# Optimization experiments

Measured on AMD Instinct MI355X. Metric: run time of the kernel, lower is better.

The kernel has to match this reference:

```python
import jax, jax.numpy as jnp
import numpy as np

B, T, D, H = 32, 4096, 768, 1024
RHOS = np.linspace(0.1, 0.9, 5)
TAU = 1.0
EPS = 1e-5


def entmax15(x):
    # exact 1.5-entmax along last axis (Peters et al. 2019)
    x = x / 2.0
    x_srt = jnp.flip(jnp.sort(x, axis=-1), axis=-1)  # descending
    n = x.shape[-1]
    rho = jnp.arange(1, n + 1, dtype=x.dtype)
    mean = jnp.cumsum(x_srt, axis=-1) / rho
    mean_sq = jnp.cumsum(x_srt * x_srt, axis=-1) / rho
    ss = rho * (mean_sq - mean * mean)
    delta = (1.0 - ss) / rho
    tau = mean - jnp.sqrt(jnp.clip(delta, 0.0))
    support = jnp.sum(tau <= x_srt, axis=-1, keepdims=True)
    tau_star = jnp.take_along_axis(tau, support - 1, axis=-1)
    return jnp.clip(x - tau_star, 0.0) ** 2


def setup_inputs() -> dict:
    key = jax.random.key(0)
    ks = jax.random.split(key, 8)
    embeddings = jax.random.normal(ks[0], (B, T, D), dtype=jnp.float32)
    ids = jax.random.randint(ks[1], (B, T), 0, 32000)
    lengths = jax.random.randint(ks[2], (B,), T // 4, T + 1)
    attn = (jnp.arange(T)[None, :] < lengths[:, None]).astype(jnp.float32)
    ln_g = jnp.ones((D,), jnp.float32)
    ln_b = jnp.zeros((D,), jnp.float32)
    W1 = 0.02 * jax.random.normal(ks[3], (D, H), dtype=jnp.float32)
    b1 = jnp.zeros((H,), jnp.float32)
    W2 = 0.02 * jax.random.normal(ks[4], (H, 1), dtype=jnp.float32)
    b2 = jnp.zeros((1,), jnp.float32)
    return {"embeddings": embeddings, "attn": attn, "ln_g": ln_g, "ln_b": ln_b,
            "W1": W1, "b1": b1, "W2": W2, "b2": b2, "ids": ids}


def reference(embeddings, attn, ln_g, ln_b, W1, b1, W2, b2, ids):
    emb = embeddings * attn[..., None]                      # [B,T,D]
    mu = jnp.mean(emb, axis=-1, keepdims=True)
    var = jnp.mean((emb - mu) ** 2, axis=-1, keepdims=True)
    xn = (emb - mu) / jnp.sqrt(var + EPS) * ln_g + ln_b
    h1 = jax.nn.gelu(xn @ W1 + b1, approximate=False)       # torch F.gelu (erf)
    scores = (h1 @ W2 + b2)[..., 0]                         # [B,T]
    scores = jnp.where(attn == 0, -1e9, scores)
    z = entmax15(scores / TAU) * attn                       # [B,T]
    sorted_idx = jnp.argsort(-z, axis=-1)                   # descending
    inv_rank = jnp.argsort(sorted_idx, axis=-1)             # rank of each position
    t_eff = jnp.sum(attn, axis=-1)                          # [B]
    rhos = jnp.asarray(RHOS, dtype=z.dtype)                 # [R]
    k = jnp.maximum(1, jnp.floor(rhos[:, None] * t_eff[None, :])).astype(jnp.int32)  # [R,B]
    h = (inv_rank[None] < k[:, :, None]).astype(z.dtype) * attn[None]  # [R,B,T]
    g = jax.lax.stop_gradient(h - z[None]) + z[None]        # straight-through
    return jnp.concatenate([z[None], g], axis=0)            # [1+R, B, T]
```

## Files before the change

### kernel.cpp

```cpp
#include <hip/hip_runtime.h>
#include <math.h>

#define Bc 32
#define Tc 4096
#define Dc 768
#define Hc 1024
#define BTc (Bc*Tc)
#define PLANE 786432

typedef __bf16 bf16x8 __attribute__((ext_vector_type(8)));
typedef float f32x16 __attribute__((ext_vector_type(16)));

__device__ __forceinline__ float gelu_erf(float x) {
  return 0.5f * x * (1.0f + erff(x * 0.70710678118654752440f));
}
__device__ __forceinline__ unsigned bf16rne(float x) {
  unsigned u = __float_as_uint(x);
  return (u + 0x7FFFu + ((u >> 16) & 1u)) >> 16;
}
__device__ __forceinline__ void split3(float x, unsigned& h, unsigned& m, unsigned& l) {
  h = bf16rne(x);
  float r1 = x - __uint_as_float(h << 16);
  m = bf16rne(r1);
  float r2 = r1 - __uint_as_float(m << 16);
  l = bf16rne(r2);
}
__device__ __forceinline__ unsigned f2o(float f) {
  unsigned b = __float_as_uint(f);
  return (b & 0x80000000u) ? ~b : (b | 0x80000000u);
}
__device__ __forceinline__ float o2f(unsigned o) {
  unsigned b = (o & 0x80000000u) ? (o & 0x7FFFFFFFu) : ~o;
  return __uint_as_float(b);
}

__global__ __launch_bounds__(256) void w1_split_k(
    const float* __restrict__ W1, ushort* __restrict__ w1s) {
  int id = blockIdx.x * 256 + threadIdx.x;
  int n = id & 1023, kg = id >> 10;
  unsigned hs[8], ms[8], ls[8];
  #pragma unroll
  for (int j = 0; j < 8; j++) {
    float x = W1[(size_t)(kg * 8 + j) * Hc + n];
    split3(x, hs[j], ms[j], ls[j]);
  }
  size_t o = ((size_t)kg * 1024 + n) * 8;
  int4 ph, pm, pl;
  ph.x = (int)(hs[0] | (hs[1] << 16)); ph.y = (int)(hs[2] | (hs[3] << 16));
  ph.z = (int)(hs[4] | (hs[5] << 16)); ph.w = (int)(hs[6] | (hs[7] << 16));
  pm.x = (int)(ms[0] | (ms[1] << 16)); pm.y = (int)(ms[2] | (ms[3] << 16));
  pm.z = (int)(ms[4] | (ms[5] << 16)); pm.w = (int)(ms[6] | (ms[7] << 16));
  pl.x = (int)(ls[0] | (ls[1] << 16)); pl.y = (int)(ls[2] | (ls[3] << 16));
  pl.z = (int)(ls[4] | (ls[5] << 16)); pl.w = (int)(ls[6] | (ls[7] << 16));
  *(int4*)(w1s + o)             = ph;
  *(int4*)(w1s + o + PLANE)     = pm;
  *(int4*)(w1s + o + 2 * PLANE) = pl;
}

__global__ __launch_bounds__(256) void ln_stats_k(
    const float* __restrict__ emb, const float* __restrict__ attn,
    float* __restrict__ mu, float* __restrict__ rstd) {
  int row = blockIdx.x * 4 + (threadIdx.x >> 6);
  int lane = threadIdx.x & 63;
  float a = attn[row];
  const float4* e = (const float4*)(emb + (size_t)row * Dc);
  float4 v0 = e[lane], v1 = e[lane + 64], v2 = e[lane + 128];
  float x[12] = {v0.x*a, v0.y*a, v0.z*a, v0.w*a,
                 v1.x*a, v1.y*a, v1.z*a, v1.w*a,
                 v2.x*a, v2.y*a, v2.z*a, v2.w*a};
  float s = 0.f;
  #pragma unroll
  for (int i = 0; i < 12; i++) s += x[i];
  #pragma unroll
  for (int o = 32; o; o >>= 1) s += __shfl_xor(s, o);
  float m = s / 768.0f;
  float q = 0.f;
  #pragma unroll
  for (int i = 0; i < 12; i++) { float d = x[i] - m; q += d * d; }
  #pragma unroll
  for (int o = 32; o; o >>= 1) q += __shfl_xor(q, o);
  float var = q / 768.0f;
  if (lane == 0) { mu[row] = m; rstd[row] = 1.0f / sqrtf(var + 1e-5f); }
}

__global__ __launch_bounds__(512, 1) void gemm_scores_mfma10(
    const float* __restrict__ emb, const float* __restrict__ attn,
    const float* __restrict__ ln_g, const float* __restrict__ ln_b,
    const ushort* __restrict__ w1s, const float* __restrict__ b1,
    const float* __restrict__ W2, const float* __restrict__ b2,
    const float* __restrict__ mu, const float* __restrict__ rstd,
    float* __restrict__ spart) {
  __shared__ int4 Abuf[2][3][4][128];
  __shared__ float gls[768], bls[768];
  __shared__ float red[8][128];
  const int id = blockIdx.x;
  const int xcd = id & 7;
  const int y = xcd & 1;
  const int xg = (id >> 3) * 4 + (xcd >> 1);
  const int base = xg * 128;
  if (attn[base] == 0.0f) return;
  const int hbase = y * 512;
  const int t = threadIdx.x;
  const int lane = t & 63;
  const int lrow = lane & 31;
  const int lkg = lane >> 5;
  const int w = t >> 6;

  if (t < 192) {
    *(float4*)&gls[t * 4] = *(const float4*)&ln_g[t * 4];
    *(float4*)&bls[t * 4] = *(const float4*)&ln_b[t * 4];
  }
  const int srow = t & 127;
  const int skg = t >> 7;
  const int skoff = skg * 8;
  const float la  = attn[base + srow];
  const float lmu = mu[base + srow];
  const float lrs = rstd[base + srow];
  const float* erow = emb + (size_t)(base + srow) * Dc + skoff;

  f32x16 acc[8];
  #pragma unroll
  for (int nt = 0; nt < 8; nt++)
    #pragma unroll
    for (int r = 0; r < 16; r++) acc[nt][r] = 0.f;

  __syncthreads();
  {
    float4 e0 = *(const float4*)(erow);
    float4 e1 = *(const float4*)(erow + 4);
    float4 g0 = *(const float4*)&gls[skoff];
    float4 g1 = *(const float4*)&gls[skoff + 4];
    float4 q0 = *(const float4*)&bls[skoff];
    float4 q1 = *(const float4*)&bls[skoff + 4];
    float xs[8] = {e0.x,e0.y,e0.z,e0.w,e1.x,e1.y,e1.z,e1.w};
    float gs[8] = {g0.x,g0.y,g0.z,g0.w,g1.x,g1.y,g1.z,g1.w};
    float bs[8] = {q0.x,q0.y,q0.z,q0.w,q1.x,q1.y,q1.z,q1.w};
    unsigned hh[8], hm[8], hl[8];
    #pragma unroll
    for (int e = 0; e < 8; e++) {
      float xn = (xs[e] * la - lmu) * lrs * gs[e] + bs[e];
      split3(xn, hh[e], hm[e], hl[e]);
    }
    int4 ph, pm, pl;
    ph.x = (int)(hh[0] | (hh[1] << 16)); ph.y = (int)(hh[2] | (hh[3] << 16));
    ph.z = (int)(hh[4] | (hh[5] << 16)); ph.w = (int)(hh[6] | (hh[7] << 16));
    pm.x = (int)(hm[0] | (hm[1] << 16)); pm.y = (int)(hm[2] | (hm[3] << 16));
    pm.z = (int)(hm[4] | (hm[5] << 16)); pm.w = (int)(hm[6] | (hm[7] << 16));
    pl.x = (int)(hl[0] | (hl[1] << 16)); pl.y = (int)(hl[2] | (hl[3] << 16));
    pl.z = (int)(hl[4] | (hl[5] << 16)); pl.w = (int)(hl[6] | (hl[7] << 16));
    Abuf[0][0][skg][srow] = ph;
    Abuf[0][1][skg][srow] = pm;
    Abuf[0][2][skg][srow] = pl;
  }
  __syncthreads();

  const ushort* wbase = w1s + ((size_t)hbase + w * 64 + lrow) * 8;

  #pragma unroll 1
  for (int i = 0; i < 24; i++) {
    const int p = i & 1;
    const bool more = (i < 23);
    #pragma unroll
    for (int kh = 0; kh < 2; kh++) {
      const int kg = kh * 2 + lkg;
      const ushort* bp = wbase + (size_t)(i * 4 + kg) * 8192;
      bf16x8 Bh0 = *(const bf16x8*)(bp);
      bf16x8 Bh1 = *(const bf16x8*)(bp + 256);
      bf16x8 Bm0 = *(const bf16x8*)(bp + PLANE);
      bf16x8 Bm1 = *(const bf16x8*)(bp + PLANE + 256);
      bf16x8 Bl0 = *(const bf16x8*)(bp + 2 * PLANE);
      bf16x8 Bl1 = *(const bf16x8*)(bp + 2 * PLANE + 256);
      #pragma unroll
      for (int rt = 0; rt < 4; rt++) {
        bf16x8 a0 = *(const bf16x8*)&Abuf[p][0][kg][rt * 32 + lrow];
        bf16x8 a1 = *(const bf16x8*)&Abuf[p][1][kg][rt * 32 + lrow];
        bf16x8 a2 = *(const bf16x8*)&Abuf[p][2][kg][rt * 32 + lrow];
        f32x16* ac = acc + rt * 2;
        ac[0] = __builtin_amdgcn_mfma_f32_32x32x16_bf16(a0, Bh0, ac[0], 0, 0, 0);
        ac[1] = __builtin_amdgcn_mfma_f32_32x32x16_bf16(a0, Bh1, ac[1], 0, 0, 0);
        ac[0] = __builtin_amdgcn_mfma_f32_32x32x16_bf16(a0, Bm0, ac[0], 0, 0, 0);
        ac[1] = __builtin_amdgcn_mfma_f32_32x32x16_bf16(a0, Bm1, ac[1], 0, 0, 0);
        ac[0] = __builtin_amdgcn_mfma_f32_32x32x16_bf16(a1, Bh0, ac[0], 0, 0, 0);
        ac[1] = __builtin_amdgcn_mfma_f32_32x32x16_bf16(a1, Bh1, ac[1], 0, 0, 0);
        ac[0] = __builtin_amdgcn_mfma_f32_32x32x16_bf16(a1, Bm0, ac[0], 0, 0, 0);
        ac[1] = __builtin_amdgcn_mfma_f32_32x32x16_bf16(a1, Bm1, ac[1], 0, 0, 0);
        ac[0] = __builtin_amdgcn_mfma_f32_32x32x16_bf16(a0, Bl0, ac[0], 0, 0, 0);
        ac[1] = __builtin_amdgcn_mfma_f32_32x32x16_bf16(a0, Bl1, ac[1], 0, 0, 0);
        ac[0] = __builtin_amdgcn_mfma_f32_32x32x16_bf16(a2, Bh0, ac[0], 0, 0, 0);
        ac[1] = __builtin_amdgcn_mfma_f32_32x32x16_bf16(a2, Bh1, ac[1], 0, 0, 0);
      }
    }
    if (more) {
      const float* ep = erow + (i + 1) * 32;
      const int koff = (i + 1) * 32 + skoff;
      float4 e0 = *(const float4*)(ep);
      float4 e1 = *(const float4*)(ep + 4);
      float4 g0 = *(const float4*)&gls[koff];
      float4 g1 = *(const float4*)&gls[koff + 4];
      float4 q0 = *(const float4*)&bls[koff];
      float4 q1 = *(const float4*)&bls[koff + 4];
      float xs[8] = {e0.x,e0.y,e0.z,e0.w,e1.x,e1.y,e1.z,e1.w};
      float gs[8] = {g0.x,g0.y,g0.z,g0.w,g1.x,g1.y,g1.z,g1.w};
      float bs[8] = {q0.x,q0.y,q0.z,q0.w,q1.x,q1.y,q1.z,q1.w};
      unsigned hh[8], hm[8], hl[8];
      #pragma unroll
      for (int e = 0; e < 8; e++) {
        float xn = (xs[e] * la - lmu) * lrs * gs[e] + bs[e];
        split3(xn, hh[e], hm[e], hl[e]);
      }
      int4 ph, pm, pl;
      ph.x = (int)(hh[0] | (hh[1] << 16)); ph.y = (int)(hh[2] | (hh[3] << 16));
      ph.z = (int)(hh[4] | (hh[5] << 16)); ph.w = (int)(hh[6] | (hh[7] << 16));
      pm.x = (int)(hm[0] | (hm[1] << 16)); pm.y = (int)(hm[2] | (hm[3] << 16));
      pm.z = (int)(hm[4] | (hm[5] << 16)); pm.w = (int)(hm[6] | (hm[7] << 16));
      pl.x = (int)(hl[0] | (hl[1] << 16)); pl.y = (int)(hl[2] | (hl[3] << 16));
      pl.z = (int)(hl[4] | (hl[5] << 16)); pl.w = (int)(hl[6] | (hl[7] << 16));
      Abuf[p ^ 1][0][skg][srow] = ph;
      Abuf[p ^ 1][1][skg][srow] = pm;
      Abuf[p ^ 1][2][skg][srow] = pl;
    }
    __syncthreads();
  }

  #pragma unroll
  for (int rt = 0; rt < 4; rt++) {
    float sacc[16];
    #pragma unroll
    for (int r = 0; r < 16; r++) sacc[r] = 0.f;
    #pragma unroll
    for (int nt = 0; nt < 2; nt++) {
      const int col = hbase + w * 64 + nt * 32 + lrow;
      const float b1v = b1[col];
      const float w2v = W2[col];
      #pragma unroll
      for (int r = 0; r < 16; r++)
        sacc[r] += gelu_erf(acc[rt * 2 + nt][r] + b1v) * w2v;
    }
    #pragma unroll
    for (int r = 0; r < 16; r++) {
      float v = sacc[r];
      v += __shfl_xor(v, 1);  v += __shfl_xor(v, 2);  v += __shfl_xor(v, 4);
      v += __shfl_xor(v, 8);  v += __shfl_xor(v, 16);
      if (lrow == 0) {
        int row = rt * 32 + (r & 3) + 8 * (r >> 2) + 4 * lkg;
        red[w][row] = v;
      }
    }
  }
  __syncthreads();
  if (t < 128) {
    float v = red[0][t] + red[1][t] + red[2][t] + red[3][t] +
              red[4][t] + red[5][t] + red[6][t] + red[7][t];
    if (y == 0) v += b2[0];
    spart[y * BTc + base + t] = v;
  }
}

__global__ __launch_bounds__(256) void entmax_rank_k(
    const float* __restrict__ sp0, const float* __restrict__ sp1,
    const float* __restrict__ attn, float* __restrict__ out) {
  const int N = 4096;
  __shared__ unsigned long long keys[4096];
  __shared__ double tsum[256], tsq[256];
  __shared__ int tcnt[256];
  __shared__ float sred[4];
  __shared__ double sh_tau;
  __shared__ int sh_S, sh_m, sh_k[5];
  const int b = blockIdx.x;
  const int t = threadIdx.x;
  const float* srow0 = sp0 + b * N;
  const float* srow1 = sp1 + b * N;
  const float* arow = attn + b * N;
  float teff_l = 0.f;
  for (int i = t; i < N; i += 256) {
    float a = arow[i];
    float s = srow0[i] + srow1[i];
    float xe = (a == 0.f) ? -1e9f : s;
    teff_l += a;
    keys[i] = ((unsigned long long)f2o(xe) << 32) |
              (unsigned long long)(0xFFFFFFFFu - (unsigned)i);
  }
  #pragma unroll
  for (int o = 32; o; o >>= 1) teff_l += __shfl_xor(teff_l, o);
  if ((t & 63) == 0) sred[t >> 6] = teff_l;
  __syncthreads();
  if (t == 0) {
    float te = sred[0] + sred[1] + sred[2] + sred[3];
    const float rh[5] = {0.1f, 0.3f, 0.5f, 0.7f, 0.9f};
    for (int r = 0; r < 5; r++) {
      int ki = (int)floorf(rh[r] * te);
      sh_k[r] = ki < 1 ? 1 : ki;
    }
  }
  for (int kk = 2; kk <= N; kk <<= 1) {
    for (int j = kk >> 1; j > 0; j >>= 1) {
      __syncthreads();
      for (int idx = t; idx < N / 2; idx += 256) {
        int i = 2 * idx - (idx & (j - 1));
        int l = i | j;
        unsigned long long A = keys[i], Bv = keys[l];
        bool up = ((i & kk) == 0);
        if (up ? (A < Bv) : (A > Bv)) { keys[i] = Bv; keys[l] = A; }
      }
    }
  }
  __syncthreads();
  const int base = t * 16;
  {
    double ls = 0, lq = 0;
    for (int ii = 0; ii < 16; ii++) {
      double x = 0.5 * (double)o2f((unsigned)(keys[base + ii] >> 32));
      ls += x; lq += x * x;
    }
    tsum[t] = ls; tsq[t] = lq;
  }
  __syncthreads();
  if (t == 0) {
    double rs = 0, rq = 0;
    for (int i = 0; i < 256; i++) {
      double a = tsum[i], c = tsq[i];
      tsum[i] = rs; tsq[i] = rq; rs += a; rq += c;
    }
  }
  __syncthreads();
  {
    double cs = tsum[t], cq = tsq[t];
    int lc = 0;
    for (int ii = 0; ii < 16; ii++) {
      double x = 0.5 * (double)o2f((unsigned)(keys[base + ii] >> 32));
      cs += x; cq += x * x;
      double rho = (double)(base + ii + 1);
      double mean = cs / rho, msq = cq / rho;
      double ss = rho * (msq - mean * mean);
      double delta = (1.0 - ss) / rho;
      double dl = delta > 0.0 ? delta : 0.0;
      double tau = mean - sqrt(dl);
      if (tau <= x) lc++;
    }
    tcnt[t] = lc;
  }
  __syncthreads();
  if (t == 0) {
    int r = 0;
    for (int i = 0; i < 256; i++) { int c = tcnt[i]; tcnt[i] = r; r += c; }
    sh_S = r;
  }
  __syncthreads();
  {
    int jstar = sh_S - 1;
    if (jstar >= base && jstar < base + 16) {
      double cs = tsum[t], cq = tsq[t], tau = 0.0;
      for (int ii = 0; ii <= jstar - base; ii++) {
        double x = 0.5 * (double)o2f((unsigned)(keys[base + ii] >> 32));
        cs += x; cq += x * x;
        double rho = (double)(base + ii + 1);
        double mean = cs / rho, msq = cq / rho;
        double ss = rho * (msq - mean * mean);
        double delta = (1.0 - ss) / rho;
        double dl = delta > 0.0 ? delta : 0.0;
        tau = mean - sqrt(dl);
      }
      sh_tau = tau;
    }
  }
  __syncthreads();
  const double tau = sh_tau;
  float ps[16], pa[16];
  {
    int lf = 0;
    for (int ii = 0; ii < 16; ii++) {
      int p = base + ii;
      ps[ii] = srow0[p] + srow1[p]; pa[ii] = arow[p];
      double d = 0.5 * (double)ps[ii] - tau;
      if (pa[ii] != 0.f && d > 0.0) lf++;
    }
    tcnt[t] = lf;
  }
  __syncthreads();
  if (t == 0) {
    int r = 0;
    for (int i = 0; i < 256; i++) { int c = tcnt[i]; tcnt[i] = r; r += c; }
    sh_m = r;
  }
  __syncthreads();
  const int m = sh_m;
  const int k0_ = sh_k[0], k1_ = sh_k[1], k2_ = sh_k[2], k3_ = sh_k[3], k4_ = sh_k[4];
  {
    int cex = tcnt[t];
    for (int ii = 0; ii < 16; ii++) {
      int p = base + ii;
      double d = 0.5 * (double)ps[ii] - tau;
      bool av = (pa[ii] != 0.f);
      bool sup = av && (d > 0.0);
      out[b * N + p] = sup ? (float)(d * d) : 0.0f;
      if (!sup) {
        int rank = m + p - cex;
        out[1 * BTc + b * N + p] = (av && rank < k0_) ? 1.f : 0.f;
        out[2 * BTc + b * N + p] = (av && rank < k1_) ? 1.f : 0.f;
        out[3 * BTc + b * N + p] = (av && rank < k2_) ? 1.f : 0.f;
        out[4 * BTc + b * N + p] = (av && rank < k3_) ? 1.f : 0.f;
        out[5 * BTc + b * N + p] = (av && rank < k4_) ? 1.f : 0.f;
      } else {
        cex++;
      }
    }
  }
  for (int r = t; r < m; r += 256) {
    int i = (int)(0xFFFFFFFFu - (unsigned)(keys[r] & 0xFFFFFFFFull));
    out[1 * BTc + b * N + i] = (r < k0_) ? 1.f : 0.f;
    out[2 * BTc + b * N + i] = (r < k1_) ? 1.f : 0.f;
    out[3 * BTc + b * N + i] = (r < k2_) ? 1.f : 0.f;
    out[4 * BTc + b * N + i] = (r < k3_) ? 1.f : 0.f;
    out[5 * BTc + b * N + i] = (r < k4_) ? 1.f : 0.f;
  }
}

extern "C" void kernel_launch(void* const* d_in, const int* in_sizes, int n_in,
                              void* d_out, int out_size, void* d_ws, size_t ws_size,
                              hipStream_t stream) {
  (void)in_sizes; (void)n_in; (void)out_size; (void)ws_size;
  const float* emb  = (const float*)d_in[0];
  const float* attn = (const float*)d_in[1];
  const float* ln_g = (const float*)d_in[2];
  const float* ln_b = (const float*)d_in[3];
  const float* W1   = (const float*)d_in[4];
  const float* b1   = (const float*)d_in[5];
  const float* W2   = (const float*)d_in[6];
  const float* b2   = (const float*)d_in[7];
  float* out = (float*)d_out;
  float* wsf = (float*)d_ws;
  float* mu     = wsf;
  float* rstd   = wsf + BTc;
  float* spart  = wsf + 2 * BTc;
  ushort* w1s   = (ushort*)(wsf + 4 * BTc);

  w1_split_k<<<384, 256, 0, stream>>>(W1, w1s);
  ln_stats_k<<<BTc / 4, 256, 0, stream>>>(emb, attn, mu, rstd);
  gemm_scores_mfma10<<<2048, 512, 0, stream>>>(
      emb, attn, ln_g, ln_b, w1s, b1, W2, b2, mu, rstd, spart);
  entmax_rank_k<<<Bc, 256, 0, stream>>>(spart, spart + BTc, attn, out);
}
```

Measured before the change: 1.100 ms.

## Split GEMM into 256-thread blocks over four H quarters for two blocks per CU

The scores GEMM now uses 256-thread blocks, each covering 128 rows by 256 hidden units, instead of 512-thread blocks covering 512 hidden units. The grid doubles and launch bounds allow two blocks per CU, so one block's barriers and LN/split staging can overlap with another block's MFMA work. Each thread now stages two k-chunks of A per step. Partial scores go into four planes that the entmax kernel sums, which adds workspace and more A-side recomputation per output column.

```diff
diff --git a/kernel.cpp b/kernel.cpp
--- a/kernel.cpp
+++ b/kernel.cpp
@@ -83,7 +83,7 @@
   if (lane == 0) { mu[row] = m; rstd[row] = 1.0f / sqrtf(var + 1e-5f); }
 }
 
-__global__ __launch_bounds__(512, 1) void gemm_scores_mfma10(
+__global__ __launch_bounds__(256, 2) void gemm_scores_mfma11(
     const float* __restrict__ emb, const float* __restrict__ attn,
     const float* __restrict__ ln_g, const float* __restrict__ ln_b,
     const ushort* __restrict__ w1s, const float* __restrict__ b1,
@@ -92,14 +92,14 @@
     float* __restrict__ spart) {
   __shared__ int4 Abuf[2][3][4][128];
   __shared__ float gls[768], bls[768];
-  __shared__ float red[8][128];
+  __shared__ float red[4][128];
   const int id = blockIdx.x;
   const int xcd = id & 7;
-  const int y = xcd & 1;
-  const int xg = (id >> 3) * 4 + (xcd >> 1);
-  const int base = xg * 128;
+  const int q = xcd & 3;
+  const int mg = (id >> 3) * 2 + (xcd >> 2);
+  const int base = mg * 128;
   if (attn[base] == 0.0f) return;
-  const int hbase = y * 512;
+  const int hbase = q * 256;
   const int t = threadIdx.x;
   const int lane = t & 63;
   const int lrow = lane & 31;
@@ -111,12 +111,11 @@
     *(float4*)&bls[t * 4] = *(const float4*)&ln_b[t * 4];
   }
   const int srow = t & 127;
-  const int skg = t >> 7;
-  const int skoff = skg * 8;
+  const int sci = t >> 7;
   const float la  = attn[base + srow];
   const float lmu = mu[base + srow];
   const float lrs = rstd[base + srow];
-  const float* erow = emb + (size_t)(base + srow) * Dc + skoff;
+  const float* erow = emb + (size_t)(base + srow) * Dc;
 
   f32x16 acc[8];
   #pragma unroll
@@ -125,13 +124,16 @@
     for (int r = 0; r < 16; r++) acc[nt][r] = 0.f;
 
   __syncthreads();
-  {
-    float4 e0 = *(const float4*)(erow);
-    float4 e1 = *(const float4*)(erow + 4);
-    float4 g0 = *(const float4*)&gls[skoff];
-    float4 g1 = *(const float4*)&gls[skoff + 4];
-    float4 q0 = *(const float4*)&bls[skoff];
-    float4 q1 = *(const float4*)&bls[skoff + 4];
+  #pragma unroll
+  for (int ci = 0; ci < 2; ci++) {
+    const int kg = sci + 2 * ci;
+    const int ko = kg * 8;
+    float4 e0 = *(const float4*)(erow + ko);
+    float4 e1 = *(const float4*)(erow + ko + 4);
+    float4 g0 = *(const float4*)&gls[ko];
+    float4 g1 = *(const float4*)&gls[ko + 4];
+    float4 q0 = *(const float4*)&bls[ko];
+    float4 q1 = *(const float4*)&bls[ko + 4];
     float xs[8] = {e0.x,e0.y,e0.z,e0.w,e1.x,e1.y,e1.z,e1.w};
     float gs[8] = {g0.x,g0.y,g0.z,g0.w,g1.x,g1.y,g1.z,g1.w};
     float bs[8] = {q0.x,q0.y,q0.z,q0.w,q1.x,q1.y,q1.z,q1.w};
@@ -148,9 +150,9 @@
     pm.z = (int)(hm[4] | (hm[5] << 16)); pm.w = (int)(hm[6] | (hm[7] << 16));
     pl.x = (int)(hl[0] | (hl[1] << 16)); pl.y = (int)(hl[2] | (hl[3] << 16));
     pl.z = (int)(hl[4] | (hl[5] << 16)); pl.w = (int)(hl[6] | (hl[7] << 16));
-    Abuf[0][0][skg][srow] = ph;
-    Abuf[0][1][skg][srow] = pm;
-    Abuf[0][2][skg][srow] = pl;
+    Abuf[0][0][kg][srow] = ph;
+    Abuf[0][1][kg][srow] = pm;
+    Abuf[0][2][kg][srow] = pl;
   }
   __syncthreads();
 
@@ -191,33 +193,36 @@
       }
     }
     if (more) {
-      const float* ep = erow + (i + 1) * 32;
-      const int koff = (i + 1) * 32 + skoff;
-      float4 e0 = *(const float4*)(ep);
-      float4 e1 = *(const float4*)(ep + 4);
-      float4 g0 = *(const float4*)&gls[koff];
-      float4 g1 = *(const float4*)&gls[koff + 4];
-      float4 q0 = *(const float4*)&bls[koff];
-      float4 q1 = *(const float4*)&bls[koff + 4];
-      float xs[8] = {e0.x,e0.y,e0.z,e0.w,e1.x,e1.y,e1.z,e1.w};
-      float gs[8] = {g0.x,g0.y,g0.z,g0.w,g1.x,g1.y,g1.z,g1.w};
-      float bs[8] = {q0.x,q0.y,q0.z,q0.w,q1.x,q1.y,q1.z,q1.w};
-      unsigned hh[8], hm[8], hl[8];
       #pragma unroll
-      for (int e = 0; e < 8; e++) {
-        float xn = (xs[e] * la - lmu) * lrs * gs[e] + bs[e];
-        split3(xn, hh[e], hm[e], hl[e]);
-      }
-      int4 ph, pm, pl;
-      ph.x = (int)(hh[0] | (hh[1] << 16)); ph.y = (int)(hh[2] | (hh[3] << 16));
-      ph.z = (int)(hh[4] | (hh[5] << 16)); ph.w = (int)(hh[6] | (hh[7] << 16));
-      pm.x = (int)(hm[0] | (hm[1] << 16)); pm.y = (int)(hm[2] | (hm[3] << 16));
-      pm.z = (int)(hm[4] | (hm[5] << 16)); pm.w = (int)(hm[6] | (hm[7] << 16));
-      pl.x = (int)(hl[0] | (hl[1] << 16)); pl.y = (int)(hl[2] | (hl[3] << 16));
-      pl.z = (int)(hl[4] | (hl[5] << 16)); pl.w = (int)(hl[6] | (hl[7] << 16));
-      Abuf[p ^ 1][0][skg][srow] = ph;
-      Abuf[p ^ 1][1][skg][srow] = pm;
-      Abuf[p ^ 1][2][skg][srow] = pl;
+      for (int ci = 0; ci < 2; ci++) {
+        const int kg = sci + 2 * ci;
+        const int ko = (i + 1) * 32 + kg * 8;
+        float4 e0 = *(const float4*)(erow + ko);
+        float4 e1 = *(const float4*)(erow + ko + 4);
+        float4 g0 = *(const float4*)&gls[ko];
+        float4 g1 = *(const float4*)&gls[ko + 4];
+        float4 q0 = *(const float4*)&bls[ko];
+        float4 q1 = *(const float4*)&bls[ko + 4];
+        float xs[8] = {e0.x,e0.y,e0.z,e0.w,e1.x,e1.y,e1.z,e1.w};
+        float gs[8] = {g0.x,g0.y,g0.z,g0.w,g1.x,g1.y,g1.z,g1.w};
+        float bs[8] = {q0.x,q0.y,q0.z,q0.w,q1.x,q1.y,q1.z,q1.w};
+        unsigned hh[8], hm[8], hl[8];
+        #pragma unroll
+        for (int e = 0; e < 8; e++) {
+          float xn = (xs[e] * la - lmu) * lrs * gs[e] + bs[e];
+          split3(xn, hh[e], hm[e], hl[e]);
+        }
+        int4 ph, pm, pl;
+        ph.x = (int)(hh[0] | (hh[1] << 16)); ph.y = (int)(hh[2] | (hh[3] << 16));
+        ph.z = (int)(hh[4] | (hh[5] << 16)); ph.w = (int)(hh[6] | (hh[7] << 16));
+        pm.x = (int)(hm[0] | (hm[1] << 16)); pm.y = (int)(hm[2] | (hm[3] << 16));
+        pm.z = (int)(hm[4] | (hm[5] << 16)); pm.w = (int)(hm[6] | (hm[7] << 16));
+        pl.x = (int)(hl[0] | (hl[1] << 16)); pl.y = (int)(hl[2] | (hl[3] << 16));
+        pl.z = (int)(hl[4] | (hl[5] << 16)); pl.w = (int)(hl[6] | (hl[7] << 16));
+        Abuf[p ^ 1][0][kg][srow] = ph;
+        Abuf[p ^ 1][1][kg][srow] = pm;
+        Abuf[p ^ 1][2][kg][srow] = pl;
+      }
     }
     __syncthreads();
   }
@@ -249,15 +254,15 @@
   }
   __syncthreads();
   if (t < 128) {
-    float v = red[0][t] + red[1][t] + red[2][t] + red[3][t] +
-              red[4][t] + red[5][t] + red[6][t] + red[7][t];
-    if (y == 0) v += b2[0];
-    spart[y * BTc + base + t] = v;
+    float v = red[0][t] + red[1][t] + red[2][t] + red[3][t];
+    if (q == 0) v += b2[0];
+    spart[q * BTc + base + t] = v;
   }
 }
 
 __global__ __launch_bounds__(256) void entmax_rank_k(
     const float* __restrict__ sp0, const float* __restrict__ sp1,
+    const float* __restrict__ sp2, const float* __restrict__ sp3,
     const float* __restrict__ attn, float* __restrict__ out) {
   const int N = 4096;
   __shared__ unsigned long long keys[4096];
@@ -270,11 +275,13 @@
   const int t = threadIdx.x;
   const float* srow0 = sp0 + b * N;
   const float* srow1 = sp1 + b * N;
+  const float* srow2 = sp2 + b * N;
+  const float* srow3 = sp3 + b * N;
   const float* arow = attn + b * N;
   float teff_l = 0.f;
   for (int i = t; i < N; i += 256) {
     float a = arow[i];
-    float s = srow0[i] + srow1[i];
+    float s = srow0[i] + srow1[i] + srow2[i] + srow3[i];
     float xe = (a == 0.f) ? -1e9f : s;
     teff_l += a;
     keys[i] = ((unsigned long long)f2o(xe) << 32) |
@@ -370,7 +377,8 @@
     int lf = 0;
     for (int ii = 0; ii < 16; ii++) {
       int p = base + ii;
-      ps[ii] = srow0[p] + srow1[p]; pa[ii] = arow[p];
+      ps[ii] = srow0[p] + srow1[p] + srow2[p] + srow3[p];
+      pa[ii] = arow[p];
       double d = 0.5 * (double)ps[ii] - tau;
       if (pa[ii] != 0.f && d > 0.0) lf++;
     }
@@ -432,11 +440,12 @@
   float* mu     = wsf;
   float* rstd   = wsf + BTc;
   float* spart  = wsf + 2 * BTc;
-  ushort* w1s   = (ushort*)(wsf + 4 * BTc);
+  ushort* w1s   = (ushort*)(wsf + 6 * BTc);
 
   w1_split_k<<<384, 256, 0, stream>>>(W1, w1s);
   ln_stats_k<<<BTc / 4, 256, 0, stream>>>(emb, attn, mu, rstd);
-  gemm_scores_mfma10<<<2048, 512, 0, stream>>>(
+  gemm_scores_mfma11<<<4096, 256, 0, stream>>>(
       emb, attn, ln_g, ln_b, w1s, b1, W2, b2, mu, rstd, spart);
-  entmax_rank_k<<<Bc, 256, 0, stream>>>(spart, spart + BTc, attn, out);
-}
+  entmax_rank_k<<<Bc, 256, 0, stream>>>(
+      spart, spart + BTc, spart + 2 * BTc, spart + 3 * BTc, attn, out);
+}
```

Measured after the change: 1.112 ms. No clear change (+1.1%).
